# Kernel tuning notes

Hardware: AMD Instinct MI355X
Metric: run time of the kernel (lower is better)

Reference implementation:

```python
import jax, jax.numpy as jnp
import numpy as np

N = 16384        # num_nodes
E = 524288       # num_edges = 32 * N
F_IN = 128
F_OUT = 128


def setup_inputs() -> dict:
    key = jax.random.key(0)
    kx, kw, ks, kd = jax.random.split(key, 4)
    x = jax.random.normal(kx, (N, F_IN), dtype=jnp.float32)
    # xavier_uniform on W of shape (out, in): bound = sqrt(6/(fan_in+fan_out))
    bound = float(np.sqrt(6.0 / (F_IN + F_OUT)))
    W = jax.random.uniform(kw, (F_OUT, F_IN), jnp.float32, -bound, bound)
    B = jnp.zeros((F_OUT, F_IN), jnp.float32)  # nn.init.zeros_
    src = jax.random.randint(ks, (E,), 0, N, dtype=jnp.int32)
    # ensure every node has at least one incoming edge (avoids 1/0 = inf degree)
    dst = jnp.concatenate([jnp.arange(N, dtype=jnp.int32),
                           jax.random.randint(kd, (E - N,), 0, N, dtype=jnp.int32)])
    edge_index = jnp.stack([src, dst], axis=0)  # [2, E]; row0=source, row1=dest
    return {"x": x, "edge_index": edge_index, "W": W, "B": B}


def reference(x, edge_index, W, B):
    n = x.shape[0]
    # dense adjacency: A[i, j] = 1 iff edge j -> i (duplicates set, not add)
    A = jnp.zeros((n, n), dtype=x.dtype).at[edge_index[1], edge_index[0]].set(1.0)
    deg = jnp.sum(A, axis=1)                      # in-degree per node, [n]
    # D^-1 A x W^T + x B^T ; diag multiply expressed as row scaling
    out = ((A @ x) / deg[:, None]) @ W.T + x @ B.T
    return out
```

## Files before the change

### kernel.cpp

```cpp
#include <hip/hip_runtime.h>
#include <cstdint>
#include <cstddef>

#define NN 16384
#define FF 128
#define CAPD 128

typedef float f32x4 __attribute__((ext_vector_type(4)));
typedef short short8 __attribute__((ext_vector_type(8)));

__device__ __forceinline__ unsigned short f2bf(float f) {
    unsigned u = __float_as_uint(f);
    u += 0x7fffu + ((u >> 16) & 1u);
    return (unsigned short)(u >> 16);
}

__device__ __forceinline__ short8 ld8(const unsigned short* p) {
    return *(const short8*)p;
}

__device__ __forceinline__ float blo(unsigned v) { return __uint_as_float(v << 16); }
__device__ __forceinline__ float bhi(unsigned v) { return __uint_as_float(v & 0xffff0000u); }

__global__ __launch_bounds__(256) void k_prep(const float4* __restrict__ x,
                                              const float4* __restrict__ W,
                                              const float4* __restrict__ B,
                                              ushort4* __restrict__ xb,
                                              ushort4* __restrict__ Wb,
                                              ushort4* __restrict__ Bb,
                                              int* __restrict__ cnt) {
    int bid = blockIdx.x;
    if (bid >= 2080) {
        cnt[(bid - 2080) * 256 + threadIdx.x] = 0;
        return;
    }
    const float4* src; ushort4* dst; int i;
    if (bid < 2048)      { src = x; dst = xb; i = bid * 256 + threadIdx.x; }
    else if (bid < 2064) { src = W; dst = Wb; i = (bid - 2048) * 256 + threadIdx.x; }
    else                 { src = B; dst = Bb; i = (bid - 2064) * 256 + threadIdx.x; }
    float4 v = src[i];
    ushort4 o;
    o.x = f2bf(v.x); o.y = f2bf(v.y); o.z = f2bf(v.z); o.w = f2bf(v.w);
    dst[i] = o;
}

__global__ __launch_bounds__(256) void k_fill(const int* __restrict__ ei,
                                              int* __restrict__ cnt,
                                              int* __restrict__ slots, int E) {
    int e = blockIdx.x * 256 + threadIdx.x;
    if (e < E) {
        int s = ei[e];
        int d = ei[E + e];
        int slot = atomicAdd(&cnt[d], 1);
        if (slot < CAPD) slots[(size_t)d * CAPD + slot] = s;
    }
}

__global__ __launch_bounds__(256) void k_agg(const int* __restrict__ cnt,
                                             const int* __restrict__ slots,
                                             const unsigned* __restrict__ xb,
                                             unsigned* __restrict__ aggs) {
    __shared__ unsigned bm[4][512];
    __shared__ int list[4][CAPD];
    __shared__ int wcnt[4];
    const int w = threadIdx.x >> 6;
    const int l = threadIdx.x & 63;
    const int i = blockIdx.x * 4 + w;
#pragma unroll
    for (int j = 0; j < 8; ++j) bm[w][l + 64 * j] = 0u;
    if (l == 0) wcnt[w] = 0;
    __syncthreads();
    int n = cnt[i]; if (n > CAPD) n = CAPD;
    const int* sl = slots + (size_t)i * CAPD;
#pragma unroll
    for (int h = 0; h < 2; ++h) {
        int j = l + 64 * h;
        if (j < n) {
            int s = sl[j];
            unsigned bit = 1u << (s & 31);
            unsigned old = atomicOr(&bm[w][s >> 5], bit);
            if (!(old & bit)) {
                int pos = atomicAdd(&wcnt[w], 1);
                list[w][pos] = s;
            }
        }
    }
    __syncthreads();
    const int deg = wcnt[w];
    const unsigned* xbl = xb + l;
    float a0 = 0.f, a1 = 0.f;
    int j = 0;
    for (; j + 8 <= deg; j += 8) {
        unsigned v0 = xbl[(size_t)list[w][j    ] * 64];
        unsigned v1 = xbl[(size_t)list[w][j + 1] * 64];
        unsigned v2 = xbl[(size_t)list[w][j + 2] * 64];
        unsigned v3 = xbl[(size_t)list[w][j + 3] * 64];
        unsigned v4 = xbl[(size_t)list[w][j + 4] * 64];
        unsigned v5 = xbl[(size_t)list[w][j + 5] * 64];
        unsigned v6 = xbl[(size_t)list[w][j + 6] * 64];
        unsigned v7 = xbl[(size_t)list[w][j + 7] * 64];
        a0 += blo(v0) + blo(v1) + blo(v2) + blo(v3)
            + blo(v4) + blo(v5) + blo(v6) + blo(v7);
        a1 += bhi(v0) + bhi(v1) + bhi(v2) + bhi(v3)
            + bhi(v4) + bhi(v5) + bhi(v6) + bhi(v7);
    }
    for (; j < deg; ++j) {
        unsigned v = xbl[(size_t)list[w][j] * 64];
        a0 += blo(v);
        a1 += bhi(v);
    }
    float inv = 1.f / (float)deg;
    unsigned o = ((unsigned)f2bf(a1 * inv) << 16) | f2bf(a0 * inv);
    aggs[(size_t)i * 64 + l] = o;
}

__global__ __launch_bounds__(256) void k_gemm(const unsigned short* __restrict__ aggs,
                                              const unsigned short* __restrict__ xb,
                                              const unsigned short* __restrict__ Wb,
                                              const unsigned short* __restrict__ Bb,
                                              float* __restrict__ out) {
    const int bid = blockIdx.x;
    const int mb = bid >> 1, nb = bid & 1;
    const int w = threadIdx.x >> 6, l = threadIdx.x & 63;
    const int row0 = mb * 64 + w * 16;
    const int col0 = nb * 64;
    const int lr = l & 15;
    const int lk = (l >> 4) * 8;

    f32x4 acc[4];
#pragma unroll
    for (int f = 0; f < 4; ++f) acc[f] = (f32x4)0.f;

#pragma unroll
    for (int p = 0; p < 2; ++p) {
        const unsigned short* A  = p ? xb : aggs;
        const unsigned short* Wt = p ? Bb : Wb;
#pragma unroll
        for (int ks = 0; ks < 4; ++ks) {
            const int k = ks * 32 + lk;
            short8 a = ld8(&A[(size_t)(row0 + lr) * FF + k]);
#pragma unroll
            for (int f = 0; f < 4; ++f) {
                short8 b = ld8(&Wt[(size_t)(col0 + f * 16 + lr) * FF + k]);
                acc[f] = __builtin_amdgcn_mfma_f32_16x16x32_bf16(a, b, acc[f], 0, 0, 0);
            }
        }
    }
#pragma unroll
    for (int f = 0; f < 4; ++f)
#pragma unroll
        for (int r = 0; r < 4; ++r)
            out[(size_t)(row0 + (l >> 4) * 4 + r) * FF + col0 + f * 16 + lr] = acc[f][r];
}

extern "C" void kernel_launch(void* const* d_in, const int* in_sizes, int n_in,
                              void* d_out, int out_size, void* d_ws, size_t ws_size,
                              hipStream_t stream) {
    const float* x = (const float*)d_in[0];
    const int* ei = (const int*)d_in[1];
    const float* W = (const float*)d_in[2];
    const float* B = (const float*)d_in[3];
    float* out = (float*)d_out;
    const int E = in_sizes[1] / 2;

    unsigned char* ws = (unsigned char*)d_ws;
    int* cnt = (int*)ws;
    int* slots = (int*)(ws + 65536);
    unsigned* xb = (unsigned*)(ws + 8454144);
    unsigned* aggs = (unsigned*)(ws + 12648448);
    unsigned short* Wb = (unsigned short*)(ws + 16842752);
    unsigned short* Bb = (unsigned short*)(ws + 16875520);

    k_prep<<<2144, 256, 0, stream>>>((const float4*)x, (const float4*)W,
                                     (const float4*)B, (ushort4*)xb,
                                     (ushort4*)Wb, (ushort4*)Bb, cnt);
    k_fill<<<(E + 255) / 256, 256, 0, stream>>>(ei, cnt, slots, E);
    k_agg<<<NN / 4, 256, 0, stream>>>(cnt, slots, xb, aggs);
    k_gemm<<<512, 256, 0, stream>>>((const unsigned short*)aggs,
                                    (const unsigned short*)xb, Wb, Bb, out);
}
```

Baseline: 62.98 us.

## Replace slot-list adjacency with global dense bitmap for dedup

Builds a per-destination dense bitmap of source nodes in global memory with atomicOr, instead of appending sources into fixed-capacity slot lists and deduplicating in shared memory. The aggregation kernel scans its 512-word row and extracts set bits into a neighbour list. This removes the per-row LDS bitmap clearing and the dedup atomics, but adds zeroing and reading a 32 MB bitmap every call.

```diff
diff --git a/kernel.cpp b/kernel.cpp
--- a/kernel.cpp
+++ b/kernel.cpp
@@ -4,7 +4,8 @@
 
 #define NN 16384
 #define FF 128
-#define CAPD 128
+#define WPR 512
+#define CAP 192
 
 typedef float f32x4 __attribute__((ext_vector_type(4)));
 typedef short short8 __attribute__((ext_vector_type(8)));
@@ -28,61 +29,58 @@
                                               ushort4* __restrict__ xb,
                                               ushort4* __restrict__ Wb,
                                               ushort4* __restrict__ Bb,
-                                              int* __restrict__ cnt) {
+                                              uint4* __restrict__ bitmap) {
     int bid = blockIdx.x;
-    if (bid >= 2080) {
-        cnt[(bid - 2080) * 256 + threadIdx.x] = 0;
+    if (bid < 2048) {
+        uint4 z = {0u, 0u, 0u, 0u};
+        uint4* p = bitmap + (size_t)bid * 1024 + threadIdx.x * 4;
+        p[0] = z; p[1] = z; p[2] = z; p[3] = z;
         return;
     }
     const float4* src; ushort4* dst; int i;
-    if (bid < 2048)      { src = x; dst = xb; i = bid * 256 + threadIdx.x; }
-    else if (bid < 2064) { src = W; dst = Wb; i = (bid - 2048) * 256 + threadIdx.x; }
-    else                 { src = B; dst = Bb; i = (bid - 2064) * 256 + threadIdx.x; }
+    if (bid < 4096)      { src = x; dst = xb; i = (bid - 2048) * 256 + threadIdx.x; }
+    else if (bid < 4112) { src = W; dst = Wb; i = (bid - 4096) * 256 + threadIdx.x; }
+    else                 { src = B; dst = Bb; i = (bid - 4112) * 256 + threadIdx.x; }
     float4 v = src[i];
     ushort4 o;
     o.x = f2bf(v.x); o.y = f2bf(v.y); o.z = f2bf(v.z); o.w = f2bf(v.w);
     dst[i] = o;
 }
 
-__global__ __launch_bounds__(256) void k_fill(const int* __restrict__ ei,
-                                              int* __restrict__ cnt,
-                                              int* __restrict__ slots, int E) {
+__global__ __launch_bounds__(256) void k_build(const int* __restrict__ ei,
+                                               unsigned* __restrict__ bitmap,
+                                               int E) {
     int e = blockIdx.x * 256 + threadIdx.x;
     if (e < E) {
         int s = ei[e];
         int d = ei[E + e];
-        int slot = atomicAdd(&cnt[d], 1);
-        if (slot < CAPD) slots[(size_t)d * CAPD + slot] = s;
+        atomicOr(&bitmap[(size_t)d * WPR + (s >> 5)], 1u << (s & 31));
     }
 }
 
-__global__ __launch_bounds__(256) void k_agg(const int* __restrict__ cnt,
-                                             const int* __restrict__ slots,
+__global__ __launch_bounds__(256) void k_agg(const unsigned* __restrict__ bitmap,
                                              const unsigned* __restrict__ xb,
                                              unsigned* __restrict__ aggs) {
-    __shared__ unsigned bm[4][512];
-    __shared__ int list[4][CAPD];
+    __shared__ int list[4][CAP];
     __shared__ int wcnt[4];
     const int w = threadIdx.x >> 6;
     const int l = threadIdx.x & 63;
     const int i = blockIdx.x * 4 + w;
-#pragma unroll
-    for (int j = 0; j < 8; ++j) bm[w][l + 64 * j] = 0u;
     if (l == 0) wcnt[w] = 0;
     __syncthreads();
-    int n = cnt[i]; if (n > CAPD) n = CAPD;
-    const int* sl = slots + (size_t)i * CAPD;
+    const unsigned* row = bitmap + (size_t)i * WPR;
+    unsigned wv[8];
 #pragma unroll
-    for (int h = 0; h < 2; ++h) {
-        int j = l + 64 * h;
-        if (j < n) {
-            int s = sl[j];
-            unsigned bit = 1u << (s & 31);
-            unsigned old = atomicOr(&bm[w][s >> 5], bit);
-            if (!(old & bit)) {
-                int pos = atomicAdd(&wcnt[w], 1);
-                list[w][pos] = s;
-            }
+    for (int j = 0; j < 8; ++j) wv[j] = row[l + 64 * j];
+#pragma unroll
+    for (int j = 0; j < 8; ++j) {
+        unsigned m = wv[j];
+        int base = (l + 64 * j) * 32;
+        while (m) {
+            int b = __ffs(m) - 1;
+            m &= m - 1;
+            int pos = atomicAdd(&wcnt[w], 1);
+            if (pos < CAP) list[w][pos] = base + b;
         }
     }
     __syncthreads();
@@ -164,18 +162,17 @@
     const int E = in_sizes[1] / 2;
 
     unsigned char* ws = (unsigned char*)d_ws;
-    int* cnt = (int*)ws;
-    int* slots = (int*)(ws + 65536);
-    unsigned* xb = (unsigned*)(ws + 8454144);
-    unsigned* aggs = (unsigned*)(ws + 12648448);
-    unsigned short* Wb = (unsigned short*)(ws + 16842752);
-    unsigned short* Bb = (unsigned short*)(ws + 16875520);
+    unsigned* bitmap = (unsigned*)ws;
+    unsigned* xb = (unsigned*)(ws + 33554432);
+    unsigned* aggs = (unsigned*)(ws + 37748736);
+    unsigned short* Wb = (unsigned short*)(ws + 41943040);
+    unsigned short* Bb = (unsigned short*)(ws + 41975808);
 
-    k_prep<<<2144, 256, 0, stream>>>((const float4*)x, (const float4*)W,
+    k_prep<<<4128, 256, 0, stream>>>((const float4*)x, (const float4*)W,
                                      (const float4*)B, (ushort4*)xb,
-                                     (ushort4*)Wb, (ushort4*)Bb, cnt);
-    k_fill<<<(E + 255) / 256, 256, 0, stream>>>(ei, cnt, slots, E);
-    k_agg<<<NN / 4, 256, 0, stream>>>(cnt, slots, xb, aggs);
+                                     (ushort4*)Wb, (ushort4*)Bb, (uint4*)bitmap);
+    k_build<<<(E + 255) / 256, 256, 0, stream>>>(ei, bitmap, E);
+    k_agg<<<NN / 4, 256, 0, stream>>>(bitmap, xb, aggs);
     k_gemm<<<512, 256, 0, stream>>>((const unsigned short*)aggs,
                                     (const unsigned short*)xb, Wb, Bb, out);
 }
```

After: 73.02 us. +15.9%, slower.
